# Optimization experiments

Hardware: AMD Instinct MI355X
Metric: run time of the kernel (lower is better)

The kernel has to match this reference:

```python
import jax, jax.numpy as jnp
import numpy as np

B, N, M, E, H = 8, 4096, 4, 512, 8
HEAD_DIM = E // H
LN_EPS = 1e-5


def setup_inputs() -> dict:
    key = jax.random.key(0)
    ks = jax.random.split(key, 12)
    inp = {}
    for i in range(M):
        inp[f"f{i}"] = jax.random.normal(ks[i], (B, N, E), dtype=jnp.float32)
    # learned query (flattened from [1,1,E])
    inp["q_param"] = jax.random.normal(ks[4], (E,), dtype=jnp.float32)
    # torch nn.MultiheadAttention packed in-projection [3E, E] and bias [3E]
    inp["in_proj_w"] = jax.random.normal(ks[5], (3 * E, E), dtype=jnp.float32) * 0.02
    inp["in_proj_b"] = jnp.zeros((3 * E,), dtype=jnp.float32)
    inp["out_proj_w"] = jax.random.normal(ks[6], (E, E), dtype=jnp.float32) * 0.02
    inp["out_proj_b"] = jnp.zeros((E,), dtype=jnp.float32)
    inp["ln_gamma"] = jnp.ones((E,), dtype=jnp.float32)
    inp["ln_beta"] = jnp.zeros((E,), dtype=jnp.float32)
    return inp


def reference(f0, f1, f2, f3, q_param, in_proj_w, in_proj_b, out_proj_w, out_proj_b, ln_gamma, ln_beta):
    x = jnp.stack([f0, f1, f2, f3], axis=2)  # [B, N, M, E]
    b, n, m, e = x.shape
    h, d = H, e // H
    scale = 1.0 / np.sqrt(d)

    Wq, Wk, Wv = jnp.split(in_proj_w, 3, axis=0)  # each [E, E]
    bq, bk, bv = jnp.split(in_proj_b, 3)

    # single learned query, shared across all (b, n) instances
    qh = ((Wq @ q_param + bq) * scale).reshape(h, d)  # [H, d]

    k = (jnp.einsum('bnme,fe->bnmf', x, Wk) + bk).reshape(b, n, m, h, d)
    v = (jnp.einsum('bnme,fe->bnmf', x, Wv) + bv).reshape(b, n, m, h, d)

    scores = jnp.einsum('hd,bnmhd->bnhm', qh, k)        # [B, N, H, M]
    attn = jax.nn.softmax(scores, axis=-1)
    o = jnp.einsum('bnhm,bnmhd->bnhd', attn, v).reshape(b, n, e)
    o = o @ out_proj_w.T + out_proj_b                   # [B, N, E]

    mu = jnp.mean(o, axis=-1, keepdims=True)
    var = jnp.var(o, axis=-1, keepdims=True)
    return (o - mu) * jax.lax.rsqrt(var + LN_EPS) * ln_gamma + ln_beta
```

## Files before the change

kernel.cpp:

```cpp
#include <hip/hip_runtime.h>
#include <hip/hip_bf16.h>


typedef float  f32x4  __attribute__((ext_vector_type(4)));
typedef float  f32x16 __attribute__((ext_vector_type(16)));
typedef short  short8 __attribute__((ext_vector_type(8)));
typedef unsigned int u32x2 __attribute__((ext_vector_type(2)));

__device__ __forceinline__ unsigned short f2bf(float f) {
  unsigned int x = __float_as_uint(f);
  unsigned int r = (x + 0x7fffu + ((x >> 16) & 1u)) >> 16;
  return (unsigned short)r;
}

__device__ __forceinline__ u32x2 pack4(const f32x4& a) {
  u32x2 r;
  asm("v_cvt_pk_bf16_f32 %0, %1, %2" : "=v"(r[0]) : "v"(a[0]), "v"(a[1]));
  asm("v_cvt_pk_bf16_f32 %0, %1, %2" : "=v"(r[1]) : "v"(a[2]), "v"(a[3]));
  return r;
}

__device__ __forceinline__ void mfma32(f32x16& c, short8 a, short8 b) {
  asm("v_mfma_f32_32x32x16_bf16 %0, %1, %2, %0" : "+v"(c) : "v"(a), "v"(b));
}
__device__ __forceinline__ void mfma16(f32x4& c, short8 a, short8 b) {
  asm("v_mfma_f32_16x16x32_bf16 %0, %1, %2, %0" : "+v"(c) : "v"(a), "v"(b));
}

__device__ __forceinline__ void gld4f(f32x4& d, const float* p) {
  asm volatile("global_load_dwordx4 %0, %1, off" : "=v"(d) : "v"(p));
}
__device__ __forceinline__ void gld4s(short8& d, const unsigned short* p) {
  asm volatile("global_load_dwordx4 %0, %1, off" : "=v"(d) : "v"(p));
}

__device__ __forceinline__ void wxv4(f32x4& a, f32x4& b, f32x4& c, f32x4& d) {
  asm volatile("s_waitcnt vmcnt(4)" : "+v"(a), "+v"(b), "+v"(c), "+v"(d));
}
__device__ __forceinline__ void wlx16(f32x4& a, f32x4& b, f32x4& c, f32x4& d,
                                      f32x4& e, f32x4& f, f32x4& g, f32x4& h) {
  asm volatile("s_waitcnt vmcnt(16)"
               : "+v"(a), "+v"(b), "+v"(c), "+v"(d),
                 "+v"(e), "+v"(f), "+v"(g), "+v"(h));
}
__device__ __forceinline__ void wbv16(short8& a, short8& b, short8& c, short8& d,
                                      short8& e, short8& f, short8& g, short8& h) {
  asm volatile("s_waitcnt vmcnt(16)"
               : "+v"(a), "+v"(b), "+v"(c), "+v"(d),
                 "+v"(e), "+v"(f), "+v"(g), "+v"(h));
}
__device__ __forceinline__ void wbv8(short8& a, short8& b, short8& c, short8& d,
                                     short8& e, short8& f, short8& g, short8& h) {
  asm volatile("s_waitcnt vmcnt(8)"
               : "+v"(a), "+v"(b), "+v"(c), "+v"(d),
                 "+v"(e), "+v"(f), "+v"(g), "+v"(h));
}
__device__ __forceinline__ void wbv0(short8& a, short8& b, short8& c, short8& d,
                                     short8& e, short8& f, short8& g, short8& h) {
  asm volatile("s_waitcnt vmcnt(0)"
               : "+v"(a), "+v"(b), "+v"(c), "+v"(d),
                 "+v"(e), "+v"(f), "+v"(g), "+v"(h));
}

__global__ void __launch_bounds__(512) tdcp_k0(
    const float* __restrict__ q_param, const float* __restrict__ in_w,
    const float* __restrict__ in_b, const float* __restrict__ out_w,
    float* __restrict__ scoreb, unsigned short* __restrict__ wscB,
    unsigned short* __restrict__ WvB, unsigned short* __restrict__ WoB)
{
  const int tid = threadIdx.x;
  const int blk = blockIdx.x;
  if (blk < 8) {
    const int h = blk;
    __shared__ float qls[512];
    __shared__ float qs[64];
    qls[tid] = q_param[tid];
    __syncthreads();
    {
      const int io = tid >> 3, sub = tid & 7;
      const float* wrow = in_w + (size_t)(h * 64 + io) * 512;
      float v = 0.f;
      #pragma unroll 8
      for (int ee = 0; ee < 64; ++ee) {
        const int e = sub + (ee << 3);
        v += wrow[e] * qls[e];
      }
      v += __shfl_xor(v, 1); v += __shfl_xor(v, 2); v += __shfl_xor(v, 4);
      if (sub == 0) qs[io] = (v + in_b[h * 64 + io]) * 0.125f;
    }
    __syncthreads();
    {
      const int e = tid;
      const float* wk = in_w + (size_t)(512 + h * 64) * 512 + e;
      float v = 0.f;
      #pragma unroll 8
      for (int jj = 0; jj < 64; ++jj) v += qs[jj] * wk[jj * 512];
      const int s32 = e >> 5, g = (e & 31) >> 3, j = e & 7;
      wscB[((s32 << 6) + h + (g << 4)) * 8 + j] = f2bf(v);
      wscB[((s32 << 6) + (h + 8) + (g << 4)) * 8 + j] = 0;
    }
    if (tid < 64) {
      float v = qs[tid] * in_b[512 + h * 64 + tid];
      v += __shfl_xor(v, 1);  v += __shfl_xor(v, 2);  v += __shfl_xor(v, 4);
      v += __shfl_xor(v, 8);  v += __shfl_xor(v, 16); v += __shfl_xor(v, 32);
      if (tid == 0) scoreb[h] = v;
    }
    if (blk == 0 && tid >= 64 && tid < 72) scoreb[tid - 56] = 0.f;
  } else {
    const int mb = blk - 8;
    const bool isWo = mb >= 64;
    const float* src = isWo ? out_w : (in_w + (size_t)1024 * 512);
    unsigned short* dst = isWo ? WoB : WvB;
    const int slot = ((mb & 63) << 9) + tid;
    const int ct = slot >> 11, kt = (slot >> 6) & 31, ln = slot & 63;
    const float* p = src + (size_t)(ct * 32 + (ln & 31)) * 512
                         + kt * 16 + ((ln >> 5) << 3);
    const f32x4 u0 = *(const f32x4*)(p);
    const f32x4 u1 = *(const f32x4*)(p + 4);
    short8 rr;
    rr[0] = (short)f2bf(u0[0]); rr[1] = (short)f2bf(u0[1]);
    rr[2] = (short)f2bf(u0[2]); rr[3] = (short)f2bf(u0[3]);
    rr[4] = (short)f2bf(u1[0]); rr[5] = (short)f2bf(u1[1]);
    rr[6] = (short)f2bf(u1[2]); rr[7] = (short)f2bf(u1[3]);
    *(short8*)(dst + slot * 8) = rr;
  }
}

__global__ void __launch_bounds__(512, 2) tdcp_k1(
    const float* __restrict__ f0, const float* __restrict__ f1,
    const float* __restrict__ f2, const float* __restrict__ f3,
    const float* __restrict__ in_b,
    const float* __restrict__ scoreb, const unsigned short* __restrict__ wscB,
    const unsigned short* __restrict__ WvB, const unsigned short* __restrict__ WoB,
    const float* __restrict__ out_b, const float* __restrict__ gamma,
    const float* __restrict__ beta, float* __restrict__ out)
{
  extern __shared__ __align__(16) char smem[];
  const int tid = threadIdx.x;
  const int w = tid >> 6;
  const int l = tid & 63;
  const int tok0 = blockIdx.x << 5;

  {
    const f32x4* wsrc = (const f32x4*)wscB;
    f32x4* wdst = (f32x4*)(smem + 65536);
    wdst[tid * 2] = wsrc[tid * 2];
    wdst[tid * 2 + 1] = wsrc[tid * 2 + 1];
  }

  const int sr = tid >> 2;
  const int c = tid & 3;
  const int sm = sr & 3;
  const int stk = sr >> 2;
  const float* fsrc = (sm == 0 ? f0 : sm == 1 ? f1 : sm == 2 ? f2 : f3)
                      + (size_t)(tok0 + stk) * 512 + (c << 2);
  int wj[4];
  #pragma unroll
  for (int j = 0; j < 4; ++j)
    wj[j] = (j << 12) + ((sr >> 5) << 10) + ((c >> 1) << 9)
          + ((((sr & 31) << 4)) ^ (j << 5)) + ((c & 1) << 3);

  const int aO = ((l >> 5) << 9) + ((l & 31) << 4);
  const int sBase = ((w >> 1) << 10) + (((l >> 4) & 1) << 9)
                  + ((((w & 1) << 4) | (l & 15)) << 4);
  const int ct0 = w << 1;
  const unsigned short* wv0 = WvB + (((ct0 * 32) << 6) + l) * 8;
  const unsigned short* wv1 = WvB + ((((ct0 + 1) * 32) << 6) + l) * 8;
  const unsigned short* wscL = (const unsigned short*)(smem + 65536);

  f32x16 acc[4][2];
  f32x4 sacc;
  #pragma unroll
  for (int i = 0; i < 4; ++i)
    #pragma unroll
    for (int cc = 0; cc < 2; ++cc)
      #pragma unroll
      for (int r = 0; r < 16; ++r) acc[i][cc][r] = 0.f;
  sacc[0] = sacc[1] = sacc[2] = sacc[3] = 0.f;

  f32x4 lx[2][4];
  short8 bb[2][8];

#define PACKSTEP(sc, bank) do {                                   \
    char* nb_ = smem + (((sc) & 3) << 14);                        \
    *(u32x2*)(nb_ + wj[0]) = pack4(lx[bank][0]);                  \
    *(u32x2*)(nb_ + wj[1]) = pack4(lx[bank][1]);                  \
    *(u32x2*)(nb_ + wj[2]) = pack4(lx[bank][2]);                  \
    *(u32x2*)(nb_ + wj[3]) = pack4(lx[bank][3]);                  \
  } while (0)

#define ISSUE_L(sc, bank) do {                                    \
    const float* p_ = fsrc + ((sc) << 6);                         \
    gld4f(lx[bank][0], p_);      gld4f(lx[bank][1], p_ + 16);     \
    gld4f(lx[bank][2], p_ + 32); gld4f(lx[bank][3], p_ + 48);     \
  } while (0)

#define ISSUE_B(sc, bank) do {                                    \
    gld4s(bb[bank][0], wv0 + ((sc) * 4 + 0) * 512);               \
    gld4s(bb[bank][1], wv1 + ((sc) * 4 + 0) * 512);               \
    gld4s(bb[bank][2], wv0 + ((sc) * 4 + 1) * 512);               \
    gld4s(bb[bank][3], wv1 + ((sc) * 4 + 1) * 512);               \
    gld4s(bb[bank][4], wv0 + ((sc) * 4 + 2) * 512);               \
    gld4s(bb[bank][5], wv1 + ((sc) * 4 + 2) * 512);               \
    gld4s(bb[bank][6], wv0 + ((sc) * 4 + 3) * 512);               \
    gld4s(bb[bank][7], wv1 + ((sc) * 4 + 3) * 512);               \
  } while (0)

#define COMPUTE(sc, bank) do {                                              \
    char* cur_ = smem + (((sc) & 3) << 14);                                 \
    const short8 sb0_ = *(const short8*)(wscL + (((2*(sc)) << 6) + l) * 8); \
    const short8 sb1_ = *(const short8*)(wscL + (((2*(sc)+1) << 6) + l) * 8);\
    __builtin_amdgcn_s_setprio(1);                                          \
    _Pragma("unroll")                                                       \
    for (int kt4 = 0; kt4 < 4; ++kt4) {                                     \
      _Pragma("unroll")                                                     \
      for (int rt = 0; rt < 4; ++rt) {                                      \
        const short8 a_ = *(const short8*)(cur_ + (kt4 << 12) + (rt << 10)  \
                                           + (aO ^ (kt4 << 5)));            \
        mfma32(acc[rt][0], a_, bb[bank][kt4 * 2]);                          \
        mfma32(acc[rt][1], a_, bb[bank][kt4 * 2 + 1]);                      \
      }                                                                     \
      if ((kt4 & 1) == 0) {                                                 \
        const int schunk_ = kt4 + (l >> 5);                                 \
        const short8 sa_ = *(const short8*)(cur_ + (schunk_ << 12)          \
                                            + (sBase ^ ((schunk_ & 3) << 5)));\
        mfma16(sacc, sa_, (kt4 == 0) ? sb0_ : sb1_);                        \
      }                                                                     \
    }                                                                       \
    __builtin_amdgcn_s_setprio(0);                                          \
  } while (0)

#define WPACK() wlx16(lx[0][0], lx[0][1], lx[0][2], lx[0][3],               \
                      lx[1][0], lx[1][1], lx[1][2], lx[1][3])
#define WB16(k) wbv16(bb[k][0], bb[k][1], bb[k][2], bb[k][3],               \
                      bb[k][4], bb[k][5], bb[k][6], bb[k][7])
#define WB8(k)  wbv8(bb[k][0], bb[k][1], bb[k][2], bb[k][3],                \
                     bb[k][4], bb[k][5], bb[k][6], bb[k][7])
#define WB0(k)  wbv0(bb[k][0], bb[k][1], bb[k][2], bb[k][3],                \
                     bb[k][4], bb[k][5], bb[k][6], bb[k][7])
#define BARRIER() do {                                            \
    asm volatile("s_waitcnt lgkmcnt(0)" ::: "memory");            \
    __builtin_amdgcn_s_barrier();                                 \
    asm volatile("" ::: "memory");                                \
  } while (0)

  ISSUE_L(0, 0); ISSUE_L(1, 1);
  wxv4(lx[0][0], lx[0][1], lx[0][2], lx[0][3]);
  PACKSTEP(0, 0);
  ISSUE_L(2, 0);
  wxv4(lx[1][0], lx[1][1], lx[1][2], lx[1][3]);
  PACKSTEP(1, 1);
  ISSUE_L(3, 1);
  ISSUE_B(0, 0); ISSUE_B(1, 1);

  BARRIER();
  WPACK();
  PACKSTEP(2, 0); PACKSTEP(3, 1);
  ISSUE_L(4, 0); ISSUE_L(5, 1);
  WB16(0);
  COMPUTE(0, 0);
  ISSUE_B(2, 0);
  WB16(1);
  COMPUTE(1, 1);
  ISSUE_B(3, 1);

  BARRIER();
  WPACK();
  PACKSTEP(4, 0); PACKSTEP(5, 1);
  ISSUE_L(6, 0); ISSUE_L(7, 1);
  WB16(0);
  COMPUTE(2, 0);
  ISSUE_B(4, 0);
  WB16(1);
  COMPUTE(3, 1);
  ISSUE_B(5, 1);

  BARRIER();
  WPACK();
  PACKSTEP(6, 0); PACKSTEP(7, 1);
  WB8(0);
  COMPUTE(4, 0);
  ISSUE_B(6, 0);
  WB8(1);
  COMPUTE(5, 1);
  ISSUE_B(7, 1);

  BARRIER();
  WB8(0);
  COMPUTE(6, 0);
  WB0(1);
  COMPUTE(7, 1);

  asm volatile("s_nop 7\n\ts_nop 7\n\ts_nop 7" ::);
  __syncthreads();

  {
    const int hh = l & 15;
    if (hh < 8) {
      const float sb = scoreb[hh];
      const float s0 = sacc[0] + sb, s1 = sacc[1] + sb;
      const float s2 = sacc[2] + sb, s3 = sacc[3] + sb;
      const float mx = fmaxf(fmaxf(s0, s1), fmaxf(s2, s3));
      const float e0 = __expf(s0 - mx), e1 = __expf(s1 - mx);
      const float e2 = __expf(s2 - mx), e3 = __expf(s3 - mx);
      const float inv = 1.f / (e0 + e1 + e2 + e3);
      f32x4 av; av[0] = e0 * inv; av[1] = e1 * inv; av[2] = e2 * inv; av[3] = e3 * inv;
      const int t = (w << 2) + (l >> 4);
      *(f32x4*)(smem + 65536 + (((t << 3) + hh) << 4)) = av;
    }
  }
  __syncthreads();

  {
    unsigned short* omid = (unsigned short*)(smem);
    #pragma unroll
    for (int c2 = 0; c2 < 2; ++c2) {
      const int ff = ((ct0 + c2) << 5) + (l & 31);
      const float bvf = in_b[1024 + ff];
      const int ktf = ff >> 4;
      const int laneL = ((l >> 3) & 1) << 5;
      const int elem = ff & 7;
      #pragma unroll
      for (int rt = 0; rt < 4; ++rt) {
        #pragma unroll
        for (int tt = 0; tt < 4; ++tt) {
          const int t = (rt << 3) + (tt << 1) + (l >> 5);
          const f32x4 av = *(const f32x4*)(smem + 65536 + (((t << 3) + w) << 4));
          const float o = av[0] * acc[rt][c2][tt * 4 + 0]
                        + av[1] * acc[rt][c2][tt * 4 + 1]
                        + av[2] * acc[rt][c2][tt * 4 + 2]
                        + av[3] * acc[rt][c2][tt * 4 + 3] + bvf;
          omid[((ktf << 6) + t + laneL) * 8 + elem] = f2bf(o);
        }
      }
    }
  }
  __syncthreads();

  f32x16 oa0, oa1;
  #pragma unroll
  for (int r = 0; r < 16; ++r) { oa0[r] = 0.f; oa1[r] = 0.f; }
  const unsigned short* wo0 = WoB + (((ct0 * 32) << 6) + l) * 8;
  const unsigned short* wo1 = WoB + ((((ct0 + 1) * 32) << 6) + l) * 8;
  const int a_off = l << 4;
  #pragma unroll 4
  for (int kt = 0; kt < 32; ++kt) {
    const short8 a = *(const short8*)(smem + (kt << 10) + a_off);
    mfma32(oa0, a, *(const short8*)(wo0 + kt * 512));
    mfma32(oa1, a, *(const short8*)(wo1 + kt * 512));
  }
  asm volatile("s_nop 7\n\ts_nop 7\n\ts_nop 7" ::);

  {
    const int g0 = (ct0 << 5) + (l & 31);
    const int g1 = g0 + 32;
    const float ob0 = out_b[g0], ob1 = out_b[g1];
    const float gm0 = gamma[g0], gm1 = gamma[g1];
    const float bt0 = beta[g0],  bt1 = beta[g1];
    float* stats = (float*)(smem + 69632);
    #pragma unroll
    for (int r = 0; r < 16; ++r) {
      const float v0 = oa0[r] + ob0, v1 = oa1[r] + ob1;
      float s = v0 + v1, qq = v0 * v0 + v1 * v1;
      s += __shfl_xor(s, 16); qq += __shfl_xor(qq, 16);
      s += __shfl_xor(s, 8);  qq += __shfl_xor(qq, 8);
      s += __shfl_xor(s, 4);  qq += __shfl_xor(qq, 4);
      s += __shfl_xor(s, 2);  qq += __shfl_xor(qq, 2);
      s += __shfl_xor(s, 1);  qq += __shfl_xor(qq, 1);
      if ((l & 31) == 0) {
        const int t = (r & 3) + ((r >> 2) << 3) + ((l >> 5) << 2);
        stats[(t << 4) + (w << 1)] = s;
        stats[(t << 4) + (w << 1) + 1] = qq;
      }
    }
    __syncthreads();
    #pragma unroll
    for (int r = 0; r < 16; ++r) {
      const int t = (r & 3) + ((r >> 2) << 3) + ((l >> 5) << 2);
      const float* st = stats + (t << 4);
      float s = 0.f, qq = 0.f;
      #pragma unroll
      for (int ww = 0; ww < 8; ++ww) { s += st[2 * ww]; qq += st[2 * ww + 1]; }
      const float mu = s * 0.001953125f;
      const float rs = rsqrtf(qq * 0.001953125f - mu * mu + 1e-5f);
      const float v0 = oa0[r] + ob0, v1 = oa1[r] + ob1;
      float* op = out + (size_t)(tok0 + t) * 512;
      op[g0] = (v0 - mu) * rs * gm0 + bt0;
      op[g1] = (v1 - mu) * rs * gm1 + bt1;
    }
  }
#undef PACKSTEP
#undef ISSUE_L
#undef ISSUE_B
#undef COMPUTE
#undef WPACK
#undef WB16
#undef WB8
#undef WB0
#undef BARRIER
}

extern "C" void kernel_launch(void* const* d_in, const int* in_sizes, int n_in,
                              void* d_out, int out_size, void* d_ws, size_t ws_size,
                              hipStream_t stream) {
  const float* f0      = (const float*)d_in[0];
  const float* f1      = (const float*)d_in[1];
  const float* f2      = (const float*)d_in[2];
  const float* f3      = (const float*)d_in[3];
  const float* q_param = (const float*)d_in[4];
  const float* in_w    = (const float*)d_in[5];
  const float* in_b    = (const float*)d_in[6];
  const float* out_w   = (const float*)d_in[7];
  const float* out_b   = (const float*)d_in[8];
  const float* gamma   = (const float*)d_in[9];
  const float* beta    = (const float*)d_in[10];
  float* out = (float*)d_out;

  char* ws = (char*)d_ws;
  float* scoreb          = (float*)ws;
  unsigned short* wscB   = (unsigned short*)(ws + 4096);
  unsigned short* WvB    = (unsigned short*)(ws + 20480);
  unsigned short* WoB    = (unsigned short*)(ws + 544768);

  hipFuncSetAttribute((const void*)tdcp_k1,
                      hipFuncAttributeMaxDynamicSharedMemorySize, 81920);

  tdcp_k0<<<136, 512, 0, stream>>>(q_param, in_w, in_b, out_w,
                                   scoreb, wscB, WvB, WoB);
  tdcp_k1<<<1024, 512, 81920, stream>>>(f0, f1, f2, f3, in_b,
                                        scoreb, wscB, WvB, WoB,
                                        out_b, gamma, beta, out);
}
```

Baseline: 161.0 us.

## Process two token groups per block with triple-buffered LDS pipeline

```diff
diff --git a/kernel.cpp b/kernel.cpp
--- a/kernel.cpp
+++ b/kernel.cpp
@@ -37,15 +37,15 @@
 __device__ __forceinline__ void wxv4(f32x4& a, f32x4& b, f32x4& c, f32x4& d) {
   asm volatile("s_waitcnt vmcnt(4)" : "+v"(a), "+v"(b), "+v"(c), "+v"(d));
 }
-__device__ __forceinline__ void wlx16(f32x4& a, f32x4& b, f32x4& c, f32x4& d,
-                                      f32x4& e, f32x4& f, f32x4& g, f32x4& h) {
-  asm volatile("s_waitcnt vmcnt(16)"
-               : "+v"(a), "+v"(b), "+v"(c), "+v"(d),
-                 "+v"(e), "+v"(f), "+v"(g), "+v"(h));
-}
-__device__ __forceinline__ void wbv16(short8& a, short8& b, short8& c, short8& d,
+__device__ __forceinline__ void wxv8(f32x4& a, f32x4& b, f32x4& c, f32x4& d) {
+  asm volatile("s_waitcnt vmcnt(8)" : "+v"(a), "+v"(b), "+v"(c), "+v"(d));
+}
+__device__ __forceinline__ void wxv12(f32x4& a, f32x4& b, f32x4& c, f32x4& d) {
+  asm volatile("s_waitcnt vmcnt(12)" : "+v"(a), "+v"(b), "+v"(c), "+v"(d));
+}
+__device__ __forceinline__ void wbv12(short8& a, short8& b, short8& c, short8& d,
                                       short8& e, short8& f, short8& g, short8& h) {
-  asm volatile("s_waitcnt vmcnt(16)"
+  asm volatile("s_waitcnt vmcnt(12)"
                : "+v"(a), "+v"(b), "+v"(c), "+v"(d),
                  "+v"(e), "+v"(f), "+v"(g), "+v"(h));
 }
@@ -135,15 +135,15 @@
     const float* __restrict__ out_b, const float* __restrict__ gamma,
     const float* __restrict__ beta, float* __restrict__ out)
 {
-  extern __shared__ __align__(16) char smem[];
+  __shared__ __align__(16) char smem[65536];
   const int tid = threadIdx.x;
   const int w = tid >> 6;
   const int l = tid & 63;
-  const int tok0 = blockIdx.x << 5;
+  const int tok0 = blockIdx.x << 6;
 
   {
     const f32x4* wsrc = (const f32x4*)wscB;
-    f32x4* wdst = (f32x4*)(smem + 65536);
+    f32x4* wdst = (f32x4*)(smem + 49152);
     wdst[tid * 2] = wsrc[tid * 2];
     wdst[tid * 2 + 1] = wsrc[tid * 2 + 1];
   }
@@ -166,51 +166,42 @@
   const int ct0 = w << 1;
   const unsigned short* wv0 = WvB + (((ct0 * 32) << 6) + l) * 8;
   const unsigned short* wv1 = WvB + ((((ct0 + 1) * 32) << 6) + l) * 8;
-  const unsigned short* wscL = (const unsigned short*)(smem + 65536);
+  const unsigned short* wscL = (const unsigned short*)(smem + 49152);
 
   f32x16 acc[4][2];
   f32x4 sacc;
-  #pragma unroll
-  for (int i = 0; i < 4; ++i)
-    #pragma unroll
-    for (int cc = 0; cc < 2; ++cc)
-      #pragma unroll
-      for (int r = 0; r < 16; ++r) acc[i][cc][r] = 0.f;
-  sacc[0] = sacc[1] = sacc[2] = sacc[3] = 0.f;
-
   f32x4 lx[2][4];
   short8 bb[2][8];
 
-#define PACKSTEP(sc, bank) do {                                   \
-    char* nb_ = smem + (((sc) & 3) << 14);                        \
+#define PACKSTEP(S, bank) do {                                    \
+    char* nb_ = smem + 16384 * ((S) % 3);                         \
     *(u32x2*)(nb_ + wj[0]) = pack4(lx[bank][0]);                  \
     *(u32x2*)(nb_ + wj[1]) = pack4(lx[bank][1]);                  \
     *(u32x2*)(nb_ + wj[2]) = pack4(lx[bank][2]);                  \
     *(u32x2*)(nb_ + wj[3]) = pack4(lx[bank][3]);                  \
   } while (0)
 
-#define ISSUE_L(sc, bank) do {                                    \
-    const float* p_ = fsrc + ((sc) << 6);                         \
+#define ISSUE_L(S, bank) do {                                     \
+    const float* p_ = fg + ((S) << 6);                            \
     gld4f(lx[bank][0], p_);      gld4f(lx[bank][1], p_ + 16);     \
     gld4f(lx[bank][2], p_ + 32); gld4f(lx[bank][3], p_ + 48);     \
   } while (0)
 
-#define ISSUE_B(sc, bank) do {                                    \
-    gld4s(bb[bank][0], wv0 + ((sc) * 4 + 0) * 512);               \
-    gld4s(bb[bank][1], wv1 + ((sc) * 4 + 0) * 512);               \
-    gld4s(bb[bank][2], wv0 + ((sc) * 4 + 1) * 512);               \
-    gld4s(bb[bank][3], wv1 + ((sc) * 4 + 1) * 512);               \
-    gld4s(bb[bank][4], wv0 + ((sc) * 4 + 2) * 512);               \
-    gld4s(bb[bank][5], wv1 + ((sc) * 4 + 2) * 512);               \
-    gld4s(bb[bank][6], wv0 + ((sc) * 4 + 3) * 512);               \
-    gld4s(bb[bank][7], wv1 + ((sc) * 4 + 3) * 512);               \
+#define ISSUE_B(S, bank) do {                                     \
+    gld4s(bb[bank][0], wv0 + ((S) * 4 + 0) * 512);                \
+    gld4s(bb[bank][1], wv1 + ((S) * 4 + 0) * 512);                \
+    gld4s(bb[bank][2], wv0 + ((S) * 4 + 1) * 512);                \
+    gld4s(bb[bank][3], wv1 + ((S) * 4 + 1) * 512);                \
+    gld4s(bb[bank][4], wv0 + ((S) * 4 + 2) * 512);                \
+    gld4s(bb[bank][5], wv1 + ((S) * 4 + 2) * 512);                \
+    gld4s(bb[bank][6], wv0 + ((S) * 4 + 3) * 512);                \
+    gld4s(bb[bank][7], wv1 + ((S) * 4 + 3) * 512);                \
   } while (0)
 
-#define COMPUTE(sc, bank) do {                                              \
-    char* cur_ = smem + (((sc) & 3) << 14);                                 \
-    const short8 sb0_ = *(const short8*)(wscL + (((2*(sc)) << 6) + l) * 8); \
-    const short8 sb1_ = *(const short8*)(wscL + (((2*(sc)+1) << 6) + l) * 8);\
-    __builtin_amdgcn_s_setprio(1);                                          \
+#define COMPUTE(S, bank) do {                                               \
+    char* cur_ = smem + 16384 * ((S) % 3);                                  \
+    const short8 sb0_ = *(const short8*)(wscL + (((2*(S)) << 6) + l) * 8);  \
+    const short8 sb1_ = *(const short8*)(wscL + (((2*(S)+1) << 6) + l) * 8);\
     _Pragma("unroll")                                                       \
     for (int kt4 = 0; kt4 < 4; ++kt4) {                                     \
       _Pragma("unroll")                                                     \
@@ -227,177 +218,179 @@
         mfma16(sacc, sa_, (kt4 == 0) ? sb0_ : sb1_);                        \
       }                                                                     \
     }                                                                       \
-    __builtin_amdgcn_s_setprio(0);                                          \
   } while (0)
 
-#define WPACK() wlx16(lx[0][0], lx[0][1], lx[0][2], lx[0][3],               \
-                      lx[1][0], lx[1][1], lx[1][2], lx[1][3])
-#define WB16(k) wbv16(bb[k][0], bb[k][1], bb[k][2], bb[k][3],               \
+#define PKW12(k) wxv12(lx[k][0], lx[k][1], lx[k][2], lx[k][3])
+#define PKW8(k)  wxv8(lx[k][0], lx[k][1], lx[k][2], lx[k][3])
+#define WB12(k)  wbv12(bb[k][0], bb[k][1], bb[k][2], bb[k][3],              \
+                       bb[k][4], bb[k][5], bb[k][6], bb[k][7])
+#define WB8(k)   wbv8(bb[k][0], bb[k][1], bb[k][2], bb[k][3],               \
                       bb[k][4], bb[k][5], bb[k][6], bb[k][7])
-#define WB8(k)  wbv8(bb[k][0], bb[k][1], bb[k][2], bb[k][3],                \
-                     bb[k][4], bb[k][5], bb[k][6], bb[k][7])
-#define WB0(k)  wbv0(bb[k][0], bb[k][1], bb[k][2], bb[k][3],                \
-                     bb[k][4], bb[k][5], bb[k][6], bb[k][7])
+#define WB0(k)   wbv0(bb[k][0], bb[k][1], bb[k][2], bb[k][3],               \
+                      bb[k][4], bb[k][5], bb[k][6], bb[k][7])
 #define BARRIER() do {                                            \
     asm volatile("s_waitcnt lgkmcnt(0)" ::: "memory");            \
     __builtin_amdgcn_s_barrier();                                 \
     asm volatile("" ::: "memory");                                \
   } while (0)
 
-  ISSUE_L(0, 0); ISSUE_L(1, 1);
-  wxv4(lx[0][0], lx[0][1], lx[0][2], lx[0][3]);
-  PACKSTEP(0, 0);
-  ISSUE_L(2, 0);
-  wxv4(lx[1][0], lx[1][1], lx[1][2], lx[1][3]);
-  PACKSTEP(1, 1);
-  ISSUE_L(3, 1);
-  ISSUE_B(0, 0); ISSUE_B(1, 1);
-
-  BARRIER();
-  WPACK();
-  PACKSTEP(2, 0); PACKSTEP(3, 1);
-  ISSUE_L(4, 0); ISSUE_L(5, 1);
-  WB16(0);
-  COMPUTE(0, 0);
-  ISSUE_B(2, 0);
-  WB16(1);
-  COMPUTE(1, 1);
-  ISSUE_B(3, 1);
-
-  BARRIER();
-  WPACK();
-  PACKSTEP(4, 0); PACKSTEP(5, 1);
-  ISSUE_L(6, 0); ISSUE_L(7, 1);
-  WB16(0);
-  COMPUTE(2, 0);
-  ISSUE_B(4, 0);
-  WB16(1);
-  COMPUTE(3, 1);
-  ISSUE_B(5, 1);
-
-  BARRIER();
-  WPACK();
-  PACKSTEP(6, 0); PACKSTEP(7, 1);
-  WB8(0);
-  COMPUTE(4, 0);
-  ISSUE_B(6, 0);
-  WB8(1);
-  COMPUTE(5, 1);
-  ISSUE_B(7, 1);
-
-  BARRIER();
-  WB8(0);
-  COMPUTE(6, 0);
-  WB0(1);
-  COMPUTE(7, 1);
-
-  asm volatile("s_nop 7\n\ts_nop 7\n\ts_nop 7" ::);
-  __syncthreads();
-
-  {
-    const int hh = l & 15;
-    if (hh < 8) {
-      const float sb = scoreb[hh];
-      const float s0 = sacc[0] + sb, s1 = sacc[1] + sb;
-      const float s2 = sacc[2] + sb, s3 = sacc[3] + sb;
-      const float mx = fmaxf(fmaxf(s0, s1), fmaxf(s2, s3));
-      const float e0 = __expf(s0 - mx), e1 = __expf(s1 - mx);
-      const float e2 = __expf(s2 - mx), e3 = __expf(s3 - mx);
-      const float inv = 1.f / (e0 + e1 + e2 + e3);
-      f32x4 av; av[0] = e0 * inv; av[1] = e1 * inv; av[2] = e2 * inv; av[3] = e3 * inv;
-      const int t = (w << 2) + (l >> 4);
-      *(f32x4*)(smem + 65536 + (((t << 3) + hh) << 4)) = av;
+#define STEP_STEADY(S)                                            \
+    PKW12((S + 1) & 1);                                           \
+    PACKSTEP((S) + 1, ((S) + 1) & 1);                             \
+    ISSUE_B((S) + 1, ((S) + 1) & 1);                              \
+    BARRIER();                                                    \
+    WB12((S) & 1);                                                \
+    COMPUTE((S), (S) & 1);
+
+  #pragma unroll 1
+  for (int g = 0; g < 2; ++g) {
+    const float* fg = fsrc + (g << 14);
+
+    #pragma unroll
+    for (int i = 0; i < 4; ++i)
+      #pragma unroll
+      for (int cc = 0; cc < 2; ++cc)
+        #pragma unroll
+        for (int r = 0; r < 16; ++r) acc[i][cc][r] = 0.f;
+    sacc[0] = sacc[1] = sacc[2] = sacc[3] = 0.f;
+
+    ISSUE_L(0, 0);
+    ISSUE_L(1, 1);
+    wxv4(lx[0][0], lx[0][1], lx[0][2], lx[0][3]);
+    PACKSTEP(0, 0);
+    ISSUE_B(0, 0);
+    ISSUE_L(2, 0);
+
+    STEP_STEADY(0); ISSUE_L(3, 1);
+    STEP_STEADY(1); ISSUE_L(4, 0);
+    STEP_STEADY(2); ISSUE_L(5, 1);
+    STEP_STEADY(3); ISSUE_L(6, 0);
+    STEP_STEADY(4); ISSUE_L(7, 1);
+    STEP_STEADY(5);
+    PKW8(1);
+    PACKSTEP(7, 1);
+    ISSUE_B(7, 1);
+    BARRIER();
+    WB8(0);
+    COMPUTE(6, 0);
+    BARRIER();
+    WB0(1);
+    COMPUTE(7, 1);
+    asm volatile("s_nop 7\n\ts_nop 7\n\ts_nop 7" ::);
+
+    const int tokG = tok0 + (g << 5);
+
+    {
+      const int hh = l & 15;
+      if (hh < 8) {
+        const float sb = scoreb[hh];
+        const float s0 = sacc[0] + sb, s1 = sacc[1] + sb;
+        const float s2 = sacc[2] + sb, s3 = sacc[3] + sb;
+        const float mx = fmaxf(fmaxf(s0, s1), fmaxf(s2, s3));
+        const float e0 = __expf(s0 - mx), e1 = __expf(s1 - mx);
+        const float e2 = __expf(s2 - mx), e3 = __expf(s3 - mx);
+        const float inv = 1.f / (e0 + e1 + e2 + e3);
+        f32x4 av; av[0] = e0 * inv; av[1] = e1 * inv;
+        av[2] = e2 * inv; av[3] = e3 * inv;
+        const int t = (w << 2) + (l >> 4);
+        *(f32x4*)(smem + 32768 + (((t << 3) + hh) << 4)) = av;
+      }
+    }
+    __syncthreads();
+
+    {
+      unsigned short* omid = (unsigned short*)(smem);
+      #pragma unroll
+      for (int c2 = 0; c2 < 2; ++c2) {
+        const int ff = ((ct0 + c2) << 5) + (l & 31);
+        const float bvf = in_b[1024 + ff];
+        const int ktf = ff >> 4;
+        const int laneL = ((l >> 3) & 1) << 5;
+        const int elem = ff & 7;
+        #pragma unroll
+        for (int rt = 0; rt < 4; ++rt) {
+          #pragma unroll
+          for (int tt = 0; tt < 4; ++tt) {
+            const int t = (rt << 3) + (tt << 1) + (l >> 5);
+            const f32x4 av = *(const f32x4*)(smem + 32768 + (((t << 3) + w) << 4));
+            const float o = av[0] * acc[rt][c2][tt * 4 + 0]
+                          + av[1] * acc[rt][c2][tt * 4 + 1]
+                          + av[2] * acc[rt][c2][tt * 4 + 2]
+                          + av[3] * acc[rt][c2][tt * 4 + 3] + bvf;
+            omid[((ktf << 6) + t + laneL) * 8 + elem] = f2bf(o);
+          }
+        }
+      }
+    }
+    __syncthreads();
+
+    f32x16 oa0, oa1;
+    #pragma unroll
+    for (int r = 0; r < 16; ++r) { oa0[r] = 0.f; oa1[r] = 0.f; }
+    {
+      const unsigned short* wo0 = WoB + (((ct0 * 32) << 6) + l) * 8;
+      const unsigned short* wo1 = WoB + ((((ct0 + 1) * 32) << 6) + l) * 8;
+      const int a_off = l << 4;
+      #pragma unroll 4
+      for (int kt = 0; kt < 32; ++kt) {
+        const short8 a = *(const short8*)(smem + (kt << 10) + a_off);
+        mfma32(oa0, a, *(const short8*)(wo0 + kt * 512));
+        mfma32(oa1, a, *(const short8*)(wo1 + kt * 512));
+      }
+    }
+    asm volatile("s_nop 7\n\ts_nop 7\n\ts_nop 7" ::);
+
+    {
+      const int g0 = (ct0 << 5) + (l & 31);
+      const int g1 = g0 + 32;
+      const float ob0 = out_b[g0], ob1 = out_b[g1];
+      const float gm0 = gamma[g0], gm1 = gamma[g1];
+      const float bt0 = beta[g0],  bt1 = beta[g1];
+      float* stats = (float*)(smem + 36864);
+      #pragma unroll
+      for (int r = 0; r < 16; ++r) {
+        const float v0 = oa0[r] + ob0, v1 = oa1[r] + ob1;
+        float s = v0 + v1, qq = v0 * v0 + v1 * v1;
+        s += __shfl_xor(s, 16); qq += __shfl_xor(qq, 16);
+        s += __shfl_xor(s, 8);  qq += __shfl_xor(qq, 8);
+        s += __shfl_xor(s, 4);  qq += __shfl_xor(qq, 4);
+        s += __shfl_xor(s, 2);  qq += __shfl_xor(qq, 2);
+        s += __shfl_xor(s, 1);  qq += __shfl_xor(qq, 1);
+        if ((l & 31) == 0) {
+          const int t = (r & 3) + ((r >> 2) << 3) + ((l >> 5) << 2);
+          stats[(t << 4) + (w << 1)] = s;
+          stats[(t << 4) + (w << 1) + 1] = qq;
+        }
+      }
+      __syncthreads();
+      #pragma unroll
+      for (int r = 0; r < 16; ++r) {
+        const int t = (r & 3) + ((r >> 2) << 3) + ((l >> 5) << 2);
+        const float* st = (const float*)(smem + 36864) + (t << 4);
+        float s = 0.f, qq = 0.f;
+        #pragma unroll
+        for (int ww = 0; ww < 8; ++ww) { s += st[2 * ww]; qq += st[2 * ww + 1]; }
+        const float mu = s * 0.001953125f;
+        const float rs = rsqrtf(qq * 0.001953125f - mu * mu + 1e-5f);
+        const float v0 = oa0[r] + ob0, v1 = oa1[r] + ob1;
+        float* op = out + (size_t)(tokG + t) * 512;
+        op[g0] = (v0 - mu) * rs * gm0 + bt0;
+        op[g1] = (v1 - mu) * rs * gm1 + bt1;
+      }
     }
   }
-  __syncthreads();
-
-  {
-    unsigned short* omid = (unsigned short*)(smem);
-    #pragma unroll
-    for (int c2 = 0; c2 < 2; ++c2) {
-      const int ff = ((ct0 + c2) << 5) + (l & 31);
-      const float bvf = in_b[1024 + ff];
-      const int ktf = ff >> 4;
-      const int laneL = ((l >> 3) & 1) << 5;
-      const int elem = ff & 7;
-      #pragma unroll
-      for (int rt = 0; rt < 4; ++rt) {
-        #pragma unroll
-        for (int tt = 0; tt < 4; ++tt) {
-          const int t = (rt << 3) + (tt << 1) + (l >> 5);
-          const f32x4 av = *(const f32x4*)(smem + 65536 + (((t << 3) + w) << 4));
-          const float o = av[0] * acc[rt][c2][tt * 4 + 0]
-                        + av[1] * acc[rt][c2][tt * 4 + 1]
-                        + av[2] * acc[rt][c2][tt * 4 + 2]
-                        + av[3] * acc[rt][c2][tt * 4 + 3] + bvf;
-          omid[((ktf << 6) + t + laneL) * 8 + elem] = f2bf(o);
-        }
-      }
-    }
-  }
-  __syncthreads();
-
-  f32x16 oa0, oa1;
-  #pragma unroll
-  for (int r = 0; r < 16; ++r) { oa0[r] = 0.f; oa1[r] = 0.f; }
-  const unsigned short* wo0 = WoB + (((ct0 * 32) << 6) + l) * 8;
-  const unsigned short* wo1 = WoB + ((((ct0 + 1) * 32) << 6) + l) * 8;
-  const int a_off = l << 4;
-  #pragma unroll 4
-  for (int kt = 0; kt < 32; ++kt) {
-    const short8 a = *(const short8*)(smem + (kt << 10) + a_off);
-    mfma32(oa0, a, *(const short8*)(wo0 + kt * 512));
-    mfma32(oa1, a, *(const short8*)(wo1 + kt * 512));
-  }
-  asm volatile("s_nop 7\n\ts_nop 7\n\ts_nop 7" ::);
-
-  {
-    const int g0 = (ct0 << 5) + (l & 31);
-    const int g1 = g0 + 32;
-    const float ob0 = out_b[g0], ob1 = out_b[g1];
-    const float gm0 = gamma[g0], gm1 = gamma[g1];
-    const float bt0 = beta[g0],  bt1 = beta[g1];
-    float* stats = (float*)(smem + 69632);
-    #pragma unroll
-    for (int r = 0; r < 16; ++r) {
-      const float v0 = oa0[r] + ob0, v1 = oa1[r] + ob1;
-      float s = v0 + v1, qq = v0 * v0 + v1 * v1;
-      s += __shfl_xor(s, 16); qq += __shfl_xor(qq, 16);
-      s += __shfl_xor(s, 8);  qq += __shfl_xor(qq, 8);
-      s += __shfl_xor(s, 4);  qq += __shfl_xor(qq, 4);
-      s += __shfl_xor(s, 2);  qq += __shfl_xor(qq, 2);
-      s += __shfl_xor(s, 1);  qq += __shfl_xor(qq, 1);
-      if ((l & 31) == 0) {
-        const int t = (r & 3) + ((r >> 2) << 3) + ((l >> 5) << 2);
-        stats[(t << 4) + (w << 1)] = s;
-        stats[(t << 4) + (w << 1) + 1] = qq;
-      }
-    }
-    __syncthreads();
-    #pragma unroll
-    for (int r = 0; r < 16; ++r) {
-      const int t = (r & 3) + ((r >> 2) << 3) + ((l >> 5) << 2);
-      const float* st = stats + (t << 4);
-      float s = 0.f, qq = 0.f;
-      #pragma unroll
-      for (int ww = 0; ww < 8; ++ww) { s += st[2 * ww]; qq += st[2 * ww + 1]; }
-      const float mu = s * 0.001953125f;
-      const float rs = rsqrtf(qq * 0.001953125f - mu * mu + 1e-5f);
-      const float v0 = oa0[r] + ob0, v1 = oa1[r] + ob1;
-      float* op = out + (size_t)(tok0 + t) * 512;
-      op[g0] = (v0 - mu) * rs * gm0 + bt0;
-      op[g1] = (v1 - mu) * rs * gm1 + bt1;
-    }
-  }
+
 #undef PACKSTEP
 #undef ISSUE_L
 #undef ISSUE_B
 #undef COMPUTE
-#undef WPACK
-#undef WB16
+#undef PKW12
+#undef PKW8
+#undef WB12
 #undef WB8
 #undef WB0
 #undef BARRIER
+#undef STEP_STEADY
 }
 
 extern "C" void kernel_launch(void* const* d_in, const int* in_sizes, int n_in,
@@ -422,12 +415,9 @@
   unsigned short* WvB    = (unsigned short*)(ws + 20480);
   unsigned short* WoB    = (unsigned short*)(ws + 544768);
 
-  hipFuncSetAttribute((const void*)tdcp_k1,
-                      hipFuncAttributeMaxDynamicSharedMemorySize, 81920);
-
   tdcp_k0<<<136, 512, 0, stream>>>(q_param, in_w, in_b, out_w,
                                    scoreb, wscB, WvB, WoB);
-  tdcp_k1<<<1024, 512, 81920, stream>>>(f0, f1, f2, f3, in_b,
-                                        scoreb, wscB, WvB, WoB,
-                                        out_b, gamma, beta, out);
-}
+  tdcp_k1<<<512, 512, 0, stream>>>(f0, f1, f2, f3, in_b,
+                                   scoreb, wscB, WvB, WoB,
+                                   out_b, gamma, beta, out);
+}
```

Measured after the change: 421.5 us. 2.62x slower.
